# Kernel tuning notes

Measured on AMD Instinct MI355X. Metric: run time of the kernel, lower is better.

## Reference

```python
import jax, jax.numpy as jnp
import numpy as np

B, L, K, D, S = 8, 1024, 1024, 128, 16  # batch, nodes, eigvecs, d_model(=d_inner), d_state
ABAR_EPS = 1e-3
BN_EPS = 1e-5


def setup_inputs() -> dict:
    key = jax.random.key(0)
    ks = jax.random.split(key, 10)
    x = jax.random.normal(ks[0], (B, L, D), jnp.float32)
    attn_mask = jnp.ones((B, L), jnp.bool_)
    EigVecs = jax.random.normal(ks[1], (B, L, K), jnp.float32)
    EigVals = jax.random.uniform(ks[2], (B, K), jnp.float32)
    # BatchNorm1d (eval mode) params
    bn_gamma = jnp.ones((D,), jnp.float32)
    bn_beta = jnp.zeros((D,), jnp.float32)
    bn_mean = jnp.zeros((D,), jnp.float32)
    bn_var = jnp.ones((D,), jnp.float32)
    # in_proj Linear(D, 2*D)
    W_in = jax.random.normal(ks[3], (D, 2 * D), jnp.float32) / np.float32(np.sqrt(D))
    b_in = jnp.zeros((2 * D,), jnp.float32)
    # SSM params
    log_Delta = np.float32(np.log(1e-3)) + np.float32(np.log(0.1) - np.log(1e-3)) * jax.random.uniform(ks[4], (1, D), jnp.float32)
    Bp = 0.01 * jax.random.normal(ks[5], (1, D, S), jnp.float32)
    Cp = 0.01 * jax.random.normal(ks[6], (1, D, S), jnp.float32)
    log_A_real = jnp.log(0.5 * jnp.ones((D, S), jnp.float32))
    A_imag = jnp.pi * jnp.broadcast_to(jnp.arange(D, dtype=jnp.float32)[:, None], (D, S))
    # out_proj Linear(D, D)
    W_out = jax.random.normal(ks[7], (D, D), jnp.float32) / np.float32(np.sqrt(D))
    b_out = jnp.zeros((D,), jnp.float32)
    return {
        "x": x, "attn_mask": attn_mask, "EigVecs": EigVecs, "EigVals": EigVals,
        "bn_gamma": bn_gamma, "bn_beta": bn_beta, "bn_mean": bn_mean, "bn_var": bn_var,
        "W_in": W_in, "b_in": b_in, "log_Delta": log_Delta, "Bp": Bp, "Cp": Cp,
        "log_A_real": log_A_real, "A_imag": A_imag, "W_out": W_out, "b_out": b_out,
    }


def reference(x, attn_mask, EigVecs, EigVals, bn_gamma, bn_beta, bn_mean, bn_var,
              W_in, b_in, log_Delta, Bp, Cp, log_A_real, A_imag, W_out, b_out):
    # --- eig preprocessing ---
    ev = 1.0 - EigVals[:, :, None, None]            # (B,K,1,1)
    ev = jnp.nan_to_num(ev)
    Q = jnp.nan_to_num(EigVecs)                      # (B,L,K)
    Q = Q / jnp.linalg.norm(Q, axis=-1, keepdims=True)
    Q = jnp.nan_to_num(Q)
    # --- in_proj: BatchNorm1d (eval) + Linear ---
    xb = (x - bn_mean) * (bn_gamma / jnp.sqrt(bn_var + BN_EPS)) + bn_beta
    h = xb @ W_in + b_in                             # (B,L,2D)
    x1, z = jnp.split(h, 2, axis=-1)                 # split [d_model, d_model]
    u = x1 * jax.nn.silu(z)                          # (B,L,D)
    # --- discretized SSM params ---
    delta = jnp.exp(log_Delta)                       # (1,D)
    A = -jnp.exp(log_A_real) + 1j * A_imag           # (D,S) complex
    Abar = jnp.exp(-ABAR_EPS + delta[..., None] * A) # (1,D,S) complex
    Bbar = delta[..., None] * Bp                     # (1,D,S)
    # --- graph Fourier transform ---
    QTX = jnp.einsum('blk,bld->bkd', Q, u)           # (B,K,D)
    QTXB = QTX[..., None] * Bbar                     # (B,K,D,S)
    lamA = ev * Abar[:, None]                        # (B,K,D,S) complex
    lamQ = jnp.real(lamA / (1.0 - lamA) * QTXB)      # A_complex & not BC_complex -> .real
    # --- inverse transform + C reduction (fused) ---
    yssm = jnp.einsum('blk,bkds,ds->bld', Q, lamQ, Cp[0])  # (B,L,D)
    y = jax.nn.silu(yssm) @ W_out + b_out
    return y
```

## Files before the change

kernel.cpp:

```cpp
#include <hip/hip_runtime.h>
#include <math.h>

#define B_ 8
#define L_ 1024
#define K_ 1024
#define D_ 128
#define S_ 16
#define DS_ (D_ * S_)
#define NIT_ 16

typedef short bf16x8 __attribute__((ext_vector_type(8)));
typedef float f32x4 __attribute__((ext_vector_type(4)));
typedef __attribute__((address_space(1))) const unsigned int gu32;
typedef __attribute__((address_space(3))) unsigned int lu32;

__device__ inline unsigned short f2bf(float f) {
    unsigned int u = __float_as_uint(f);
    u = (u + 0x7fffu + ((u >> 16) & 1u)) >> 16;
    return (unsigned short)u;
}
__device__ inline float bf2f(unsigned short h) {
    return __uint_as_float(((unsigned int)h) << 16);
}

__device__ inline size_t bswz(int b, int c, int n) {
    return ((((size_t)b * 32 + (c >> 5)) * 4 + ((c >> 3) & 3)) * 128 + n) * 8;
}

__global__ __launch_bounds__(256) void k_w(
    const float* __restrict__ W_in,
    unsigned short* __restrict__ wiH, unsigned short* __restrict__ wiL) {
    int g = blockIdx.x * 256 + threadIdx.x;
    int lane = g & 63, rest = g >> 6;
    int ct = rest & 3, wv = (rest >> 2) & 3, c = rest >> 4;
    int rbase = c * 32 + (lane >> 4) * 8;
    int col = wv * 64 + ct * 16 + (lane & 15);
    bf16x8 hv, lv;
    #pragma unroll
    for (int i = 0; i < 8; ++i) {
        float wvl = W_in[(rbase + i) * 256 + col];
        unsigned short h = f2bf(wvl);
        hv[i] = (short)h;
        lv[i] = (short)f2bf(wvl - bf2f(h));
    }
    *(bf16x8*)&wiH[(size_t)g * 8] = hv;
    *(bf16x8*)&wiL[(size_t)g * 8] = lv;
}

__global__ __launch_bounds__(256) void k_pre(
    const float* __restrict__ E, const float* __restrict__ x,
    const float* __restrict__ g, const float* __restrict__ beta,
    const float* __restrict__ mean, const float* __restrict__ var,
    const unsigned short* __restrict__ wiH, const unsigned short* __restrict__ wiL,
    const float* __restrict__ b_in,
    const float* __restrict__ log_Delta, const float* __restrict__ Bp,
    const float* __restrict__ Cp, const float* __restrict__ log_A_real,
    const float* __restrict__ A_imag, const float* __restrict__ W_out,
    float* __restrict__ rn_out, float* __restrict__ par,
    unsigned short* __restrict__ woH, unsigned short* __restrict__ woL,
    unsigned short* __restrict__ uswH, unsigned short* __restrict__ uswL) {
    __shared__ unsigned short xbh[4][16][32], xbl[4][16][32];
    __shared__ float szs[16][132];
    __shared__ float us[16][132];
    __shared__ float rsum[16];
    __shared__ float rnS[16];
    int bx = blockIdx.x;
    int row0 = bx * 16;
    int t = threadIdx.x;
    if (bx < 8) {
        int i = bx * 256 + t;
        int d = i >> 4, s = i & 15;
        double delta = exp((double)log_Delta[d]);
        double Are = -exp((double)log_A_real[i]);
        double Aim = (double)A_imag[i];
        double mag = exp(-1e-3 + delta * Are);
        double ang = delta * Aim;
        int o = s * D_ + d;
        par[o]           = (float)(mag * cos(ang));
        par[DS_ + o]     = (float)(mag * sin(ang));
        par[2 * DS_ + o] = (float)(delta * (double)Bp[i] * (double)Cp[i]);
    }
    if (bx >= 8 && bx < 12) {
        int kc = bx - 8;
        #pragma unroll
        for (int j = 0; j < 16; ++j) {
            int s = t * 16 + j;
            int ws = s >> 10, nt = (s >> 9) & 1, ln = (s >> 3) & 63, ii = s & 7;
            int row = kc * 32 + (ln >> 4) * 8 + ii;
            int col = ws * 32 + nt * 16 + (ln & 15);
            float wv = W_out[row * 128 + col];
            unsigned short h = f2bf(wv);
            woH[kc * 4096 + s] = h;
            woL[kc * 4096 + s] = f2bf(wv - bf2f(h));
        }
    }
    {
        int r = t >> 4, tt = t & 15;
        const float4* Ep = (const float4*)(E + (size_t)(row0 + r) * K_);
        float s = 0.f;
        #pragma unroll
        for (int i = 0; i < 16; ++i) {
            float4 v = Ep[tt + i * 16];
            s += v.x * v.x + v.y * v.y + v.z * v.z + v.w * v.w;
        }
        s += __shfl_xor(s, 8, 64);
        s += __shfl_xor(s, 4, 64);
        s += __shfl_xor(s, 2, 64);
        s += __shfl_xor(s, 1, 64);
        if (tt == 0) rsum[r] = s;
    }
    #pragma unroll
    for (int p = 0; p < 8; ++p) {
        int idx = t + p * 256;
        int dd = idx & 127, r = idx >> 7;
        float sc = g[dd] / sqrtf(var[dd] + 1e-5f);
        float v = (x[(size_t)(row0 + r) * D_ + dd] - mean[dd]) * sc + beta[dd];
        unsigned short h = f2bf(v);
        xbh[dd >> 5][r][dd & 31] = h;
        xbl[dd >> 5][r][dd & 31] = f2bf(v - bf2f(h));
    }
    __syncthreads();
    if (t < 16) {
        float rv = 1.0f / sqrtf(rsum[t]);
        rnS[t] = rv;
        rn_out[row0 + t] = rv;
    }
    __syncthreads();
    int wave = t >> 6, lane = t & 63;
    int fr = lane & 15, q = lane >> 4;
    const bf16x8* WIH = (const bf16x8*)wiH;
    const bf16x8* WIL = (const bf16x8*)wiL;
    f32x4 acc[4];
    #pragma unroll
    for (int ct = 0; ct < 4; ++ct) acc[ct] = (f32x4){0.f, 0.f, 0.f, 0.f};
    #pragma unroll
    for (int c = 0; c < 4; ++c) {
        bf16x8 ah = *(const bf16x8*)&xbh[c][fr][q * 8];
        bf16x8 al = *(const bf16x8*)&xbl[c][fr][q * 8];
        #pragma unroll
        for (int ct = 0; ct < 4; ++ct) {
            int idx = ((c * 4 + wave) * 4 + ct) * 64 + lane;
            bf16x8 bh = WIH[idx];
            bf16x8 bl = WIL[idx];
            acc[ct] = __builtin_amdgcn_mfma_f32_16x16x32_bf16(ah, bh, acc[ct], 0, 0, 0);
            acc[ct] = __builtin_amdgcn_mfma_f32_16x16x32_bf16(ah, bl, acc[ct], 0, 0, 0);
            acc[ct] = __builtin_amdgcn_mfma_f32_16x16x32_bf16(al, bh, acc[ct], 0, 0, 0);
        }
    }
    if (wave >= 2) {
        #pragma unroll
        for (int ct = 0; ct < 4; ++ct) {
            int cz = (wave - 2) * 64 + ct * 16 + fr;
            float b2v = b_in[128 + cz];
            #pragma unroll
            for (int r = 0; r < 4; ++r) {
                float z = acc[ct][r] + b2v;
                float sig = 1.0f / (1.0f + __expf(-z));
                szs[q * 4 + r][cz] = z * sig;
            }
        }
    }
    __syncthreads();
    if (wave < 2) {
        #pragma unroll
        for (int ct = 0; ct < 4; ++ct) {
            int cx = wave * 64 + ct * 16 + fr;
            float b1v = b_in[cx];
            #pragma unroll
            for (int r = 0; r < 4; ++r) {
                int row = q * 4 + r;
                float x1 = acc[ct][r] + b1v;
                us[row][cx] = rnS[row] * x1 * szs[row][cx];
            }
        }
    }
    __syncthreads();
    int j = t & 127, half = t >> 7;
    bf16x8 hv, lv;
    #pragma unroll
    for (int r = 0; r < 8; ++r) {
        float uv = us[half * 8 + r][j];
        unsigned short h = f2bf(uv);
        hv[r] = (short)h;
        lv[r] = (short)f2bf(uv - bf2f(h));
    }
    int b = row0 >> 10;
    int l0 = (row0 & 1023) + half * 8;
    size_t off = bswz(b, l0, j);
    *(bf16x8*)&uswH[off] = hv;
    *(bf16x8*)&uswL[off] = lv;
}

#define STAGE_B(itS, nb)                                                        \
    _Pragma("unroll")                                                           \
    for (int j2 = 0; j2 < 4; ++j2) {                                            \
        int s = wave * 4 + j2;                         \
        int cts = s >> 4, s2 = s & 15;                                          \
        int qq = s2 & 3, nh = (s2 >> 2) & 1, hl = s2 >> 3;                      \
        size_t src0 = (size_t)((itS) * 2 + cts) * 4096;                         \
        const unsigned short* src =                                             \
            (hl ? BbL : BbH) + src0 + ((size_t)qq * 128 + nh * 64 + lane) * 8;  \
        unsigned short* dst =                                                   \
            (hl ? &sBl[nb][cts][0] : &sBh[nb][cts][0]) + qq * 1032 + nh * 512;  \
        __builtin_amdgcn_global_load_lds((gu32*)src, (lu32*)dst, 16, 0, 0);     \
    }

#define G1_WRITE_A(nb, v0, v1, v2, v3)                                           \
    {                                                                            \
        unsigned short h0 = f2bf(v0), h1 = f2bf(v1);                             \
        unsigned short l0 = f2bf((v0) - bf2f(h0)), l1 = f2bf((v1) - bf2f(h1));   \
        *(unsigned int*)&sAh[nb][0][aoff] = (unsigned)h0 | ((unsigned)h1 << 16); \
        *(unsigned int*)&sAl[nb][0][aoff] = (unsigned)l0 | ((unsigned)l1 << 16); \
        unsigned short h2 = f2bf(v2), h3 = f2bf(v3);                             \
        unsigned short l2 = f2bf((v2) - bf2f(h2)), l3 = f2bf((v3) - bf2f(h3));   \
        *(unsigned int*)&sAh[nb][1][aoff] = (unsigned)h2 | ((unsigned)h3 << 16); \
        *(unsigned int*)&sAl[nb][1][aoff] = (unsigned)l2 | ((unsigned)l3 << 16); \
    }

#define MFMA_PHASE(aB, cB)                                                       \
    {                                                                            \
        __builtin_amdgcn_s_setprio(1);                                           \
        bf16x8 ah[2], al[2], bh[2], bl[2];                                       \
        _Pragma("unroll")                                                        \
        for (int mt = 0; mt < 2; ++mt) {                                         \
            int row = mt * 16 + fr;                                              \
            int p = (q + (row >> 3)) & 3;                                        \
            int offA = row * 40 + p * 8;                                         \
            ah[mt] = *(const bf16x8*)&sAh[aB][kh][offA];                         \
            al[mt] = *(const bf16x8*)&sAl[aB][kh][offA];                         \
        }                                                                        \
        _Pragma("unroll")                                                        \
        for (int nt = 0; nt < 2; ++nt) {                                         \
            int offB = q * 1032 + (wn + nt * 16 + fr) * 8;                       \
            bh[nt] = *(const bf16x8*)&sBh[cB][kh][offB];                         \
            bl[nt] = *(const bf16x8*)&sBl[cB][kh][offB];                         \
        }                                                                        \
        _Pragma("unroll")                                                        \
        for (int mt = 0; mt < 2; ++mt)                                           \
            _Pragma("unroll")                                                    \
            for (int nt = 0; nt < 2; ++nt) {                                     \
                acc[mt][nt] = __builtin_amdgcn_mfma_f32_16x16x32_bf16(ah[mt], bh[nt], acc[mt][nt], 0, 0, 0); \
                acc[mt][nt] = __builtin_amdgcn_mfma_f32_16x16x32_bf16(ah[mt], bl[nt], acc[mt][nt], 0, 0, 0); \
                acc[mt][nt] = __builtin_amdgcn_mfma_f32_16x16x32_bf16(al[mt], bh[nt], acc[mt][nt], 0, 0, 0); \
            }                                                                    \
        __builtin_amdgcn_s_setprio(0);                                           \
    }

__global__ __launch_bounds__(512, 2) void k_g1(
    const float* __restrict__ E,
    const unsigned short* __restrict__ BH, const unsigned short* __restrict__ BL,
    const float* __restrict__ EigVals, const float* __restrict__ par,
    unsigned short* __restrict__ GswH, unsigned short* __restrict__ GswL) {
    __shared__ alignas(16) unsigned short sAh[2][2][1280], sAl[2][2][1280];
    __shared__ alignas(16) unsigned short sBh[3][2][4128], sBl[3][2][4128];
    __shared__ float evS[32];
    int bx = blockIdx.x;
    int b = bx & 7;
    int m0 = (bx >> 3) * 32;
    const float* Ab = E + (size_t)b * (1024 * 1024);
    const unsigned short* BbH = BH + (size_t)b * 131072;
    const unsigned short* BbL = BL + (size_t)b * 131072;
    int t = threadIdx.x;
    int wave = t >> 6, lane = t & 63;
    int fr = lane & 15, q = lane >> 4;
    int kh = wave & 1;
    int wn = (wave >> 1) * 32;
    int am = t & 31, jj = t >> 5;
    int ag = jj >> 2;
    int arot = (ag + (am >> 3)) & 3;
    int aoff = am * 40 + arot * 8 + ((2 * jj) & 7);
    if (t < 32) evS[t] = 1.0f - EigVals[b * 1024 + m0 + t];
    f32x4 acc[2][2];
    #pragma unroll
    for (int mt = 0; mt < 2; ++mt)
        #pragma unroll
        for (int nt = 0; nt < 2; ++nt)
            acc[mt][nt] = (f32x4){0.f, 0.f, 0.f, 0.f};

    {
        STAGE_B(0, 0);
        STAGE_B(1, 1);
        float v0 = Ab[(size_t)(2 * jj) * 1024 + m0 + am];
        float v1 = Ab[(size_t)(2 * jj + 1) * 1024 + m0 + am];
        float v2 = Ab[(size_t)(32 + 2 * jj) * 1024 + m0 + am];
        float v3 = Ab[(size_t)(32 + 2 * jj + 1) * 1024 + m0 + am];
        G1_WRITE_A(0, v0, v1, v2, v3);
        asm volatile("s_waitcnt vmcnt(0) lgkmcnt(0)" ::: "memory");
        __builtin_amdgcn_s_barrier();
        asm volatile("" ::: "memory");
    }

    for (int it = 0; it < NIT_; ++it) {
        int cB = it % 3;
        int fB = (it + 2) % 3;
        int aB = it & 1, naB = aB ^ 1;
        float v0 = 0.f, v1 = 0.f, v2 = 0.f, v3 = 0.f;
        if (it + 1 < NIT_) {
            int cb = (it + 1) * 64;
            v0 = Ab[(size_t)(cb + 2 * jj) * 1024 + m0 + am];
            v1 = Ab[(size_t)(cb + 2 * jj + 1) * 1024 + m0 + am];
            v2 = Ab[(size_t)(cb + 32 + 2 * jj) * 1024 + m0 + am];
            v3 = Ab[(size_t)(cb + 32 + 2 * jj + 1) * 1024 + m0 + am];
        }
        if (it + 2 < NIT_) STAGE_B(it + 2, fB);
        MFMA_PHASE(aB, cB)
        if (it + 1 < NIT_) G1_WRITE_A(naB, v0, v1, v2, v3);
        asm volatile("s_waitcnt lgkmcnt(0)" ::: "memory");
        __builtin_amdgcn_s_barrier();
        asm volatile("" ::: "memory");
    }

    float (*Gs)[132] = (float (*)[132])(&sBh[0][0][0]);
    if (kh == 0) {
        #pragma unroll
        for (int mt = 0; mt < 2; ++mt)
            #pragma unroll
            for (int nt = 0; nt < 2; ++nt) {
                int col = wn + nt * 16 + fr;
                #pragma unroll
                for (int r = 0; r < 4; ++r)
                    Gs[mt * 16 + q * 4 + r][col] = acc[mt][nt][r];
            }
    }
    __syncthreads();
    if (kh == 1) {
        #pragma unroll
        for (int mt = 0; mt < 2; ++mt)
            #pragma unroll
            for (int nt = 0; nt < 2; ++nt) {
                int col = wn + nt * 16 + fr;
                #pragma unroll
                for (int r = 0; r < 4; ++r)
                    Gs[mt * 16 + q * 4 + r][col] += acc[mt][nt][r];
            }
    }
    __syncthreads();
    {
        int col = t & 127, rowg = t >> 7;
        float arr[S_], aii[S_], ccc[S_];
        #pragma unroll
        for (int ss = 0; ss < S_; ++ss) {
            arr[ss] = par[ss * D_ + col];
            aii[ss] = par[DS_ + ss * D_ + col];
            ccc[ss] = par[2 * DS_ + ss * D_ + col];
        }
        #pragma unroll
        for (int i = 0; i < 8; ++i) {
            int row = rowg * 8 + i;
            float ev = evS[row];
            float w = 0.f;
            #pragma unroll
            for (int sp = 0; sp < 8; ++sp) {
                float n0, n1, d0, d1;
                {
                    int ss = sp * 2;
                    float a = ev * arr[ss], bi = ev * aii[ss];
                    float oma = 1.0f - a;
                    d0 = fmaf(oma, oma, bi * bi);
                    n0 = ccc[ss] * (oma - d0);
                }
                {
                    int ss = sp * 2 + 1;
                    float a = ev * arr[ss], bi = ev * aii[ss];
                    float oma = 1.0f - a;
                    d1 = fmaf(oma, oma, bi * bi);
                    n1 = ccc[ss] * (oma - d1);
                }
                float num = fmaf(n0, d1, n1 * d0);
                float dpr = d0 * d1;
                float rr = __builtin_amdgcn_rcpf(dpr);
                rr = rr * (2.0f - dpr * rr);
                w = fmaf(num, rr, w);
            }
            Gs[row][col] *= w;
        }
    }
    __syncthreads();
    {
        int d = t & 127, kg = t >> 7;
        bf16x8 hv, lv;
        #pragma unroll
        for (int i = 0; i < 8; ++i) {
            float v = Gs[kg * 8 + i][d];
            unsigned short h = f2bf(v);
            hv[i] = (short)h;
            lv[i] = (short)f2bf(v - bf2f(h));
        }
        int ct = m0 >> 5;
        size_t off = (((size_t)(b * 32 + ct) * 4 + kg) * 128 + d) * 8;
        *(bf16x8*)&GswH[off] = hv;
        *(bf16x8*)&GswL[off] = lv;
    }
}

#define G2_WRITE_A(nb, va)                                                       \
    {                                                                            \
        unsigned short h0 = f2bf((va).x), h1 = f2bf((va).y);                     \
        unsigned short h2 = f2bf((va).z), h3 = f2bf((va).w);                     \
        unsigned short l0 = f2bf((va).x - bf2f(h0)), l1 = f2bf((va).y - bf2f(h1));\
        unsigned short l2 = f2bf((va).z - bf2f(h2)), l3 = f2bf((va).w - bf2f(h3));\
        *(uint2*)&sAh[nb][chunk][aoff] =                                         \
            (uint2){(unsigned)h0 | ((unsigned)h1 << 16),                         \
                    (unsigned)h2 | ((unsigned)h3 << 16)};                        \
        *(uint2*)&sAl[nb][chunk][aoff] =                                         \
            (uint2){(unsigned)l0 | ((unsigned)l1 << 16),                         \
                    (unsigned)l2 | ((unsigned)l3 << 16)};                        \
    }

__global__ __launch_bounds__(512, 2) void k_g2(
    const float* __restrict__ E,
    const unsigned short* __restrict__ BH, const unsigned short* __restrict__ BL,
    const float* __restrict__ rn,
    const unsigned short* __restrict__ woH, const unsigned short* __restrict__ woL,
    const float* __restrict__ b_out, float* __restrict__ y) {
    __shared__ alignas(16) unsigned short sAh[2][2][1280], sAl[2][2][1280];
    __shared__ alignas(16) unsigned short sBh[3][2][4128], sBl[3][2][4128];
    __shared__ float rnS[32];
    int bx = blockIdx.x;
    int b = bx & 7;
    int m0 = (bx >> 3) * 32;
    const float* Ab = E + (size_t)b * (1024 * 1024);
    const unsigned short* BbH = BH + (size_t)b * 131072;
    const unsigned short* BbL = BL + (size_t)b * 131072;
    int t = threadIdx.x;
    int wave = t >> 6, lane = t & 63;
    int fr = lane & 15, q = lane >> 4;
    int kh = wave & 1;
    int wn = (wave >> 1) * 32;
    int am = t >> 4, c4 = (t & 15) * 4;
    int chunk = c4 >> 5, cw = c4 & 31;
    int ag = cw >> 3;
    int arot = (ag + (am >> 3)) & 3;
    int aoff = am * 40 + arot * 8 + (cw & 7);
    if (t < 32) rnS[t] = rn[b * 1024 + m0 + t];
    f32x4 acc[2][2];
    #pragma unroll
    for (int mt = 0; mt < 2; ++mt)
        #pragma unroll
        for (int nt = 0; nt < 2; ++nt)
            acc[mt][nt] = (f32x4){0.f, 0.f, 0.f, 0.f};

    {
        STAGE_B(0, 0);
        STAGE_B(1, 1);
        float4 va = *(const float4*)&Ab[(size_t)(m0 + am) * 1024 + c4];
        G2_WRITE_A(0, va);
        asm volatile("s_waitcnt vmcnt(0) lgkmcnt(0)" ::: "memory");
        __builtin_amdgcn_s_barrier();
        asm volatile("" ::: "memory");
    }

    for (int it = 0; it < NIT_; ++it) {
        int cB = it % 3;
        int fB = (it + 2) % 3;
        int aB = it & 1, naB = aB ^ 1;
        float4 va = (float4){0.f, 0.f, 0.f, 0.f};
        if (it + 1 < NIT_)
            va = *(const float4*)&Ab[(size_t)(m0 + am) * 1024 + (it + 1) * 64 + c4];
        if (it + 2 < NIT_) STAGE_B(it + 2, fB);
        MFMA_PHASE(aB, cB)
        if (it + 1 < NIT_) G2_WRITE_A(naB, va);
        asm volatile("s_waitcnt lgkmcnt(0)" ::: "memory");
        __builtin_amdgcn_s_barrier();
        asm volatile("" ::: "memory");
    }

    float (*Ysf)[132] = (float (*)[132])(&sBh[0][0][0]);
    if (kh == 0) {
        #pragma unroll
        for (int mt = 0; mt < 2; ++mt)
            #pragma unroll
            for (int nt = 0; nt < 2; ++nt) {
                int col = wn + nt * 16 + fr;
                #pragma unroll
                for (int r = 0; r < 4; ++r)
                    Ysf[mt * 16 + q * 4 + r][col] = acc[mt][nt][r];
            }
    }
    __syncthreads();
    if (kh == 1) {
        #pragma unroll
        for (int mt = 0; mt < 2; ++mt)
            #pragma unroll
            for (int nt = 0; nt < 2; ++nt) {
                int col = wn + nt * 16 + fr;
                #pragma unroll
                for (int r = 0; r < 4; ++r)
                    Ysf[mt * 16 + q * 4 + r][col] += acc[mt][nt][r];
            }
    }
    __syncthreads();
    unsigned short (*ysh)[32][40] = (unsigned short (*)[32][40])(&sBl[0][0][0]);
    unsigned short (*ysl)[32][40] = (unsigned short (*)[32][40])(&sBl[0][0][0] + 5120);
    {
        int col = t & 127, rowg = t >> 7;
        #pragma unroll
        for (int i = 0; i < 8; ++i) {
            int row = rowg * 8 + i;
            float v = Ysf[row][col] * rnS[row];
            float sig = 1.0f / (1.0f + __expf(-v));
            float u = v * sig;
            unsigned short h = f2bf(u);
            ysh[col >> 5][row][col & 31] = h;
            ysl[col >> 5][row][col & 31] = f2bf(u - bf2f(h));
        }
    }
    __syncthreads();
    {
        int mh = wave & 1, ws = wave >> 1;
        const bf16x8* WH = (const bf16x8*)woH;
        const bf16x8* WL = (const bf16x8*)woL;
        f32x4 a2[2];
        a2[0] = (f32x4){0.f, 0.f, 0.f, 0.f};
        a2[1] = (f32x4){0.f, 0.f, 0.f, 0.f};
        #pragma unroll
        for (int kc = 0; kc < 4; ++kc) {
            bf16x8 ah = *(const bf16x8*)&ysh[kc][mh * 16 + fr][q * 8];
            bf16x8 al = *(const bf16x8*)&ysl[kc][mh * 16 + fr][q * 8];
            #pragma unroll
            for (int nt = 0; nt < 2; ++nt) {
                bf16x8 bh = WH[((kc * 4 + ws) * 2 + nt) * 64 + lane];
                bf16x8 bl = WL[((kc * 4 + ws) * 2 + nt) * 64 + lane];
                a2[nt] = __builtin_amdgcn_mfma_f32_16x16x32_bf16(ah, bh, a2[nt], 0, 0, 0);
                a2[nt] = __builtin_amdgcn_mfma_f32_16x16x32_bf16(ah, bl, a2[nt], 0, 0, 0);
                a2[nt] = __builtin_amdgcn_mfma_f32_16x16x32_bf16(al, bh, a2[nt], 0, 0, 0);
            }
        }
        #pragma unroll
        for (int nt = 0; nt < 2; ++nt) {
            int col = ws * 32 + nt * 16 + fr;
            float bo = b_out[col];
            #pragma unroll
            for (int r = 0; r < 4; ++r) {
                int row = mh * 16 + q * 4 + r;
                y[((size_t)b * 1024 + m0 + row) * 128 + col] = a2[nt][r] + bo;
            }
        }
    }
}

extern "C" void kernel_launch(void* const* d_in, const int* in_sizes, int n_in,
                              void* d_out, int out_size, void* d_ws, size_t ws_size,
                              hipStream_t stream) {
    const float* x          = (const float*)d_in[0];
    const float* EigVecs    = (const float*)d_in[2];
    const float* EigVals    = (const float*)d_in[3];
    const float* bn_gamma   = (const float*)d_in[4];
    const float* bn_beta    = (const float*)d_in[5];
    const float* bn_mean    = (const float*)d_in[6];
    const float* bn_var     = (const float*)d_in[7];
    const float* W_in       = (const float*)d_in[8];
    const float* b_in       = (const float*)d_in[9];
    const float* log_Delta  = (const float*)d_in[10];
    const float* Bp         = (const float*)d_in[11];
    const float* Cp         = (const float*)d_in[12];
    const float* log_A_real = (const float*)d_in[13];
    const float* A_imag     = (const float*)d_in[14];
    const float* W_out      = (const float*)d_in[15];
    const float* b_out      = (const float*)d_in[16];

    float* y = (float*)d_out;
    char* w = (char*)d_ws;
    float* rn            = (float*)(w);
    float* par           = (float*)(w + 32768);
    unsigned short* woH  = (unsigned short*)(w + 57344);
    unsigned short* woL  = (unsigned short*)(w + 90112);
    unsigned short* wiH  = (unsigned short*)(w + 131072);
    unsigned short* wiL  = (unsigned short*)(w + 196608);
    unsigned short* uswH = (unsigned short*)(w + 262144);
    unsigned short* uswL = (unsigned short*)(w + 262144 + (1u << 21));
    unsigned short* GswH = (unsigned short*)(w + 262144 + 2 * (1u << 21));
    unsigned short* GswL = (unsigned short*)(w + 262144 + 3 * (1u << 21));

    k_w<<<dim3(16), dim3(256), 0, stream>>>(W_in, wiH, wiL);
    k_pre<<<dim3(B_ * L_ / 16), dim3(256), 0, stream>>>(
        EigVecs, x, bn_gamma, bn_beta, bn_mean, bn_var, wiH, wiL, b_in,
        log_Delta, Bp, Cp, log_A_real, A_imag, W_out, rn, par, woH, woL,
        uswH, uswL);
    k_g1<<<dim3(256), dim3(512), 0, stream>>>(
        EigVecs, uswH, uswL, EigVals, par, GswH, GswL);
    k_g2<<<dim3(256), dim3(512), 0, stream>>>(
        EigVecs, GswH, GswL, rn, woH, woL, b_out, y);
}
```

Baseline: 152.3 us.

## Merge the two GEMM kernels into one cooperative kernel with a grid sync

Fuses k_g1 (the forward graph transform plus spectral filter) and k_g2 (the inverse transform plus out_proj) into a single cooperative kernel. A grid-wide barrier separates the two phases. The first A tile of the second phase is prefetched before the barrier. The aim is to remove one kernel launch and its drain/fill gap and to hide some load latency. In exchange it adds the cost of a grid sync, and it relies on all 256 blocks of 512 threads being co-resident.

```diff
diff --git a/kernel.cpp b/kernel.cpp
--- a/kernel.cpp
+++ b/kernel.cpp
@@ -1,5 +1,8 @@
 #include <hip/hip_runtime.h>
+#include <hip/hip_cooperative_groups.h>
 #include <math.h>
+
+namespace cg = cooperative_groups;
 
 #define B_ 8
 #define L_ 1024
@@ -246,153 +249,6 @@
         __builtin_amdgcn_s_setprio(0);                                           \
     }
 
-__global__ __launch_bounds__(512, 2) void k_g1(
-    const float* __restrict__ E,
-    const unsigned short* __restrict__ BH, const unsigned short* __restrict__ BL,
-    const float* __restrict__ EigVals, const float* __restrict__ par,
-    unsigned short* __restrict__ GswH, unsigned short* __restrict__ GswL) {
-    __shared__ alignas(16) unsigned short sAh[2][2][1280], sAl[2][2][1280];
-    __shared__ alignas(16) unsigned short sBh[3][2][4128], sBl[3][2][4128];
-    __shared__ float evS[32];
-    int bx = blockIdx.x;
-    int b = bx & 7;
-    int m0 = (bx >> 3) * 32;
-    const float* Ab = E + (size_t)b * (1024 * 1024);
-    const unsigned short* BbH = BH + (size_t)b * 131072;
-    const unsigned short* BbL = BL + (size_t)b * 131072;
-    int t = threadIdx.x;
-    int wave = t >> 6, lane = t & 63;
-    int fr = lane & 15, q = lane >> 4;
-    int kh = wave & 1;
-    int wn = (wave >> 1) * 32;
-    int am = t & 31, jj = t >> 5;
-    int ag = jj >> 2;
-    int arot = (ag + (am >> 3)) & 3;
-    int aoff = am * 40 + arot * 8 + ((2 * jj) & 7);
-    if (t < 32) evS[t] = 1.0f - EigVals[b * 1024 + m0 + t];
-    f32x4 acc[2][2];
-    #pragma unroll
-    for (int mt = 0; mt < 2; ++mt)
-        #pragma unroll
-        for (int nt = 0; nt < 2; ++nt)
-            acc[mt][nt] = (f32x4){0.f, 0.f, 0.f, 0.f};
-
-    {
-        STAGE_B(0, 0);
-        STAGE_B(1, 1);
-        float v0 = Ab[(size_t)(2 * jj) * 1024 + m0 + am];
-        float v1 = Ab[(size_t)(2 * jj + 1) * 1024 + m0 + am];
-        float v2 = Ab[(size_t)(32 + 2 * jj) * 1024 + m0 + am];
-        float v3 = Ab[(size_t)(32 + 2 * jj + 1) * 1024 + m0 + am];
-        G1_WRITE_A(0, v0, v1, v2, v3);
-        asm volatile("s_waitcnt vmcnt(0) lgkmcnt(0)" ::: "memory");
-        __builtin_amdgcn_s_barrier();
-        asm volatile("" ::: "memory");
-    }
-
-    for (int it = 0; it < NIT_; ++it) {
-        int cB = it % 3;
-        int fB = (it + 2) % 3;
-        int aB = it & 1, naB = aB ^ 1;
-        float v0 = 0.f, v1 = 0.f, v2 = 0.f, v3 = 0.f;
-        if (it + 1 < NIT_) {
-            int cb = (it + 1) * 64;
-            v0 = Ab[(size_t)(cb + 2 * jj) * 1024 + m0 + am];
-            v1 = Ab[(size_t)(cb + 2 * jj + 1) * 1024 + m0 + am];
-            v2 = Ab[(size_t)(cb + 32 + 2 * jj) * 1024 + m0 + am];
-            v3 = Ab[(size_t)(cb + 32 + 2 * jj + 1) * 1024 + m0 + am];
-        }
-        if (it + 2 < NIT_) STAGE_B(it + 2, fB);
-        MFMA_PHASE(aB, cB)
-        if (it + 1 < NIT_) G1_WRITE_A(naB, v0, v1, v2, v3);
-        asm volatile("s_waitcnt lgkmcnt(0)" ::: "memory");
-        __builtin_amdgcn_s_barrier();
-        asm volatile("" ::: "memory");
-    }
-
-    float (*Gs)[132] = (float (*)[132])(&sBh[0][0][0]);
-    if (kh == 0) {
-        #pragma unroll
-        for (int mt = 0; mt < 2; ++mt)
-            #pragma unroll
-            for (int nt = 0; nt < 2; ++nt) {
-                int col = wn + nt * 16 + fr;
-                #pragma unroll
-                for (int r = 0; r < 4; ++r)
-                    Gs[mt * 16 + q * 4 + r][col] = acc[mt][nt][r];
-            }
-    }
-    __syncthreads();
-    if (kh == 1) {
-        #pragma unroll
-        for (int mt = 0; mt < 2; ++mt)
-            #pragma unroll
-            for (int nt = 0; nt < 2; ++nt) {
-                int col = wn + nt * 16 + fr;
-                #pragma unroll
-                for (int r = 0; r < 4; ++r)
-                    Gs[mt * 16 + q * 4 + r][col] += acc[mt][nt][r];
-            }
-    }
-    __syncthreads();
-    {
-        int col = t & 127, rowg = t >> 7;
-        float arr[S_], aii[S_], ccc[S_];
-        #pragma unroll
-        for (int ss = 0; ss < S_; ++ss) {
-            arr[ss] = par[ss * D_ + col];
-            aii[ss] = par[DS_ + ss * D_ + col];
-            ccc[ss] = par[2 * DS_ + ss * D_ + col];
-        }
-        #pragma unroll
-        for (int i = 0; i < 8; ++i) {
-            int row = rowg * 8 + i;
-            float ev = evS[row];
-            float w = 0.f;
-            #pragma unroll
-            for (int sp = 0; sp < 8; ++sp) {
-                float n0, n1, d0, d1;
-                {
-                    int ss = sp * 2;
-                    float a = ev * arr[ss], bi = ev * aii[ss];
-                    float oma = 1.0f - a;
-                    d0 = fmaf(oma, oma, bi * bi);
-                    n0 = ccc[ss] * (oma - d0);
-                }
-                {
-                    int ss = sp * 2 + 1;
-                    float a = ev * arr[ss], bi = ev * aii[ss];
-                    float oma = 1.0f - a;
-                    d1 = fmaf(oma, oma, bi * bi);
-                    n1 = ccc[ss] * (oma - d1);
-                }
-                float num = fmaf(n0, d1, n1 * d0);
-                float dpr = d0 * d1;
-                float rr = __builtin_amdgcn_rcpf(dpr);
-                rr = rr * (2.0f - dpr * rr);
-                w = fmaf(num, rr, w);
-            }
-            Gs[row][col] *= w;
-        }
-    }
-    __syncthreads();
-    {
-        int d = t & 127, kg = t >> 7;
-        bf16x8 hv, lv;
-        #pragma unroll
-        for (int i = 0; i < 8; ++i) {
-            float v = Gs[kg * 8 + i][d];
-            unsigned short h = f2bf(v);
-            hv[i] = (short)h;
-            lv[i] = (short)f2bf(v - bf2f(h));
-        }
-        int ct = m0 >> 5;
-        size_t off = (((size_t)(b * 32 + ct) * 4 + kg) * 128 + d) * 8;
-        *(bf16x8*)&GswH[off] = hv;
-        *(bf16x8*)&GswL[off] = lv;
-    }
-}
-
 #define G2_WRITE_A(nb, va)                                                       \
     {                                                                            \
         unsigned short h0 = f2bf((va).x), h1 = f2bf((va).y);                     \
@@ -407,133 +263,275 @@
                     (unsigned)l2 | ((unsigned)l3 << 16)};                        \
     }
 
-__global__ __launch_bounds__(512, 2) void k_g2(
+__global__ __launch_bounds__(512, 2) void k_gg(
     const float* __restrict__ E,
-    const unsigned short* __restrict__ BH, const unsigned short* __restrict__ BL,
+    const unsigned short* __restrict__ uswH, const unsigned short* __restrict__ uswL,
+    const float* __restrict__ EigVals, const float* __restrict__ par,
+    unsigned short* __restrict__ GswH, unsigned short* __restrict__ GswL,
     const float* __restrict__ rn,
     const unsigned short* __restrict__ woH, const unsigned short* __restrict__ woL,
     const float* __restrict__ b_out, float* __restrict__ y) {
     __shared__ alignas(16) unsigned short sAh[2][2][1280], sAl[2][2][1280];
     __shared__ alignas(16) unsigned short sBh[3][2][4128], sBl[3][2][4128];
+    __shared__ float evS[32];
     __shared__ float rnS[32];
     int bx = blockIdx.x;
     int b = bx & 7;
     int m0 = (bx >> 3) * 32;
     const float* Ab = E + (size_t)b * (1024 * 1024);
-    const unsigned short* BbH = BH + (size_t)b * 131072;
-    const unsigned short* BbL = BL + (size_t)b * 131072;
     int t = threadIdx.x;
     int wave = t >> 6, lane = t & 63;
     int fr = lane & 15, q = lane >> 4;
     int kh = wave & 1;
     int wn = (wave >> 1) * 32;
-    int am = t >> 4, c4 = (t & 15) * 4;
-    int chunk = c4 >> 5, cw = c4 & 31;
-    int ag = cw >> 3;
-    int arot = (ag + (am >> 3)) & 3;
-    int aoff = am * 40 + arot * 8 + (cw & 7);
+
+    {
+        const unsigned short* BbH = uswH + (size_t)b * 131072;
+        const unsigned short* BbL = uswL + (size_t)b * 131072;
+        int am = t & 31, jj = t >> 5;
+        int ag = jj >> 2;
+        int arot = (ag + (am >> 3)) & 3;
+        int aoff = am * 40 + arot * 8 + ((2 * jj) & 7);
+        if (t < 32) evS[t] = 1.0f - EigVals[b * 1024 + m0 + t];
+        f32x4 acc[2][2];
+        #pragma unroll
+        for (int mt = 0; mt < 2; ++mt)
+            #pragma unroll
+            for (int nt = 0; nt < 2; ++nt)
+                acc[mt][nt] = (f32x4){0.f, 0.f, 0.f, 0.f};
+
+        {
+            STAGE_B(0, 0);
+            STAGE_B(1, 1);
+            float v0 = Ab[(size_t)(2 * jj) * 1024 + m0 + am];
+            float v1 = Ab[(size_t)(2 * jj + 1) * 1024 + m0 + am];
+            float v2 = Ab[(size_t)(32 + 2 * jj) * 1024 + m0 + am];
+            float v3 = Ab[(size_t)(32 + 2 * jj + 1) * 1024 + m0 + am];
+            G1_WRITE_A(0, v0, v1, v2, v3);
+            asm volatile("s_waitcnt vmcnt(0) lgkmcnt(0)" ::: "memory");
+            __builtin_amdgcn_s_barrier();
+            asm volatile("" ::: "memory");
+        }
+
+        for (int it = 0; it < NIT_; ++it) {
+            int cB = it % 3;
+            int fB = (it + 2) % 3;
+            int aB = it & 1, naB = aB ^ 1;
+            float v0 = 0.f, v1 = 0.f, v2 = 0.f, v3 = 0.f;
+            if (it + 1 < NIT_) {
+                int cb = (it + 1) * 64;
+                v0 = Ab[(size_t)(cb + 2 * jj) * 1024 + m0 + am];
+                v1 = Ab[(size_t)(cb + 2 * jj + 1) * 1024 + m0 + am];
+                v2 = Ab[(size_t)(cb + 32 + 2 * jj) * 1024 + m0 + am];
+                v3 = Ab[(size_t)(cb + 32 + 2 * jj + 1) * 1024 + m0 + am];
+            }
+            if (it + 2 < NIT_) STAGE_B(it + 2, fB);
+            MFMA_PHASE(aB, cB)
+            if (it + 1 < NIT_) G1_WRITE_A(naB, v0, v1, v2, v3);
+            asm volatile("s_waitcnt lgkmcnt(0)" ::: "memory");
+            __builtin_amdgcn_s_barrier();
+            asm volatile("" ::: "memory");
+        }
+
+        float (*Gs)[132] = (float (*)[132])(&sBh[0][0][0]);
+        if (kh == 0) {
+            #pragma unroll
+            for (int mt = 0; mt < 2; ++mt)
+                #pragma unroll
+                for (int nt = 0; nt < 2; ++nt) {
+                    int col = wn + nt * 16 + fr;
+                    #pragma unroll
+                    for (int r = 0; r < 4; ++r)
+                        Gs[mt * 16 + q * 4 + r][col] = acc[mt][nt][r];
+                }
+        }
+        __syncthreads();
+        if (kh == 1) {
+            #pragma unroll
+            for (int mt = 0; mt < 2; ++mt)
+                #pragma unroll
+                for (int nt = 0; nt < 2; ++nt) {
+                    int col = wn + nt * 16 + fr;
+                    #pragma unroll
+                    for (int r = 0; r < 4; ++r)
+                        Gs[mt * 16 + q * 4 + r][col] += acc[mt][nt][r];
+                }
+        }
+        __syncthreads();
+        {
+            int col = t & 127, rowg = t >> 7;
+            float arr[S_], aii[S_], ccc[S_];
+            #pragma unroll
+            for (int ss = 0; ss < S_; ++ss) {
+                arr[ss] = par[ss * D_ + col];
+                aii[ss] = par[DS_ + ss * D_ + col];
+                ccc[ss] = par[2 * DS_ + ss * D_ + col];
+            }
+            #pragma unroll
+            for (int i = 0; i < 8; ++i) {
+                int row = rowg * 8 + i;
+                float ev = evS[row];
+                float w = 0.f;
+                #pragma unroll
+                for (int sp = 0; sp < 8; ++sp) {
+                    float n0, n1, d0, d1;
+                    {
+                        int ss = sp * 2;
+                        float a = ev * arr[ss], bi = ev * aii[ss];
+                        float oma = 1.0f - a;
+                        d0 = fmaf(oma, oma, bi * bi);
+                        n0 = ccc[ss] * (oma - d0);
+                    }
+                    {
+                        int ss = sp * 2 + 1;
+                        float a = ev * arr[ss], bi = ev * aii[ss];
+                        float oma = 1.0f - a;
+                        d1 = fmaf(oma, oma, bi * bi);
+                        n1 = ccc[ss] * (oma - d1);
+                    }
+                    float num = fmaf(n0, d1, n1 * d0);
+                    float dpr = d0 * d1;
+                    float rr = __builtin_amdgcn_rcpf(dpr);
+                    rr = rr * (2.0f - dpr * rr);
+                    w = fmaf(num, rr, w);
+                }
+                Gs[row][col] *= w;
+            }
+        }
+        __syncthreads();
+        {
+            int d = t & 127, kg = t >> 7;
+            bf16x8 hv, lv;
+            #pragma unroll
+            for (int i = 0; i < 8; ++i) {
+                float v = Gs[kg * 8 + i][d];
+                unsigned short h = f2bf(v);
+                hv[i] = (short)h;
+                lv[i] = (short)f2bf(v - bf2f(h));
+            }
+            int ct = m0 >> 5;
+            size_t off = (((size_t)(b * 32 + ct) * 4 + kg) * 128 + d) * 8;
+            *(bf16x8*)&GswH[off] = hv;
+            *(bf16x8*)&GswL[off] = lv;
+        }
+    }
+
+    int am2 = t >> 4, c42 = (t & 15) * 4;
+    float4 va0 = *(const float4*)&Ab[(size_t)(m0 + am2) * 1024 + c42];
     if (t < 32) rnS[t] = rn[b * 1024 + m0 + t];
-    f32x4 acc[2][2];
-    #pragma unroll
-    for (int mt = 0; mt < 2; ++mt)
-        #pragma unroll
-        for (int nt = 0; nt < 2; ++nt)
-            acc[mt][nt] = (f32x4){0.f, 0.f, 0.f, 0.f};
+
+    __threadfence();
+    cg::this_grid().sync();
 
     {
-        STAGE_B(0, 0);
-        STAGE_B(1, 1);
-        float4 va = *(const float4*)&Ab[(size_t)(m0 + am) * 1024 + c4];
-        G2_WRITE_A(0, va);
-        asm volatile("s_waitcnt vmcnt(0) lgkmcnt(0)" ::: "memory");
-        __builtin_amdgcn_s_barrier();
-        asm volatile("" ::: "memory");
-    }
-
-    for (int it = 0; it < NIT_; ++it) {
-        int cB = it % 3;
-        int fB = (it + 2) % 3;
-        int aB = it & 1, naB = aB ^ 1;
-        float4 va = (float4){0.f, 0.f, 0.f, 0.f};
-        if (it + 1 < NIT_)
-            va = *(const float4*)&Ab[(size_t)(m0 + am) * 1024 + (it + 1) * 64 + c4];
-        if (it + 2 < NIT_) STAGE_B(it + 2, fB);
-        MFMA_PHASE(aB, cB)
-        if (it + 1 < NIT_) G2_WRITE_A(naB, va);
-        asm volatile("s_waitcnt lgkmcnt(0)" ::: "memory");
-        __builtin_amdgcn_s_barrier();
-        asm volatile("" ::: "memory");
-    }
-
-    float (*Ysf)[132] = (float (*)[132])(&sBh[0][0][0]);
-    if (kh == 0) {
+        const unsigned short* BbH = GswH + (size_t)b * 131072;
+        const unsigned short* BbL = GswL + (size_t)b * 131072;
+        int am = am2, c4 = c42;
+        int chunk = c4 >> 5, cw = c4 & 31;
+        int ag = cw >> 3;
+        int arot = (ag + (am >> 3)) & 3;
+        int aoff = am * 40 + arot * 8 + (cw & 7);
+        f32x4 acc[2][2];
         #pragma unroll
         for (int mt = 0; mt < 2; ++mt)
             #pragma unroll
+            for (int nt = 0; nt < 2; ++nt)
+                acc[mt][nt] = (f32x4){0.f, 0.f, 0.f, 0.f};
+
+        {
+            STAGE_B(0, 0);
+            STAGE_B(1, 1);
+            G2_WRITE_A(0, va0);
+            asm volatile("s_waitcnt vmcnt(0) lgkmcnt(0)" ::: "memory");
+            __builtin_amdgcn_s_barrier();
+            asm volatile("" ::: "memory");
+        }
+
+        for (int it = 0; it < NIT_; ++it) {
+            int cB = it % 3;
+            int fB = (it + 2) % 3;
+            int aB = it & 1, naB = aB ^ 1;
+            float4 va = (float4){0.f, 0.f, 0.f, 0.f};
+            if (it + 1 < NIT_)
+                va = *(const float4*)&Ab[(size_t)(m0 + am) * 1024 + (it + 1) * 64 + c4];
+            if (it + 2 < NIT_) STAGE_B(it + 2, fB);
+            MFMA_PHASE(aB, cB)
+            if (it + 1 < NIT_) G2_WRITE_A(naB, va);
+            asm volatile("s_waitcnt lgkmcnt(0)" ::: "memory");
+            __builtin_amdgcn_s_barrier();
+            asm volatile("" ::: "memory");
+        }
+
+        float (*Ysf)[132] = (float (*)[132])(&sBh[0][0][0]);
+        if (kh == 0) {
+            #pragma unroll
+            for (int mt = 0; mt < 2; ++mt)
+                #pragma unroll
+                for (int nt = 0; nt < 2; ++nt) {
+                    int col = wn + nt * 16 + fr;
+                    #pragma unroll
+                    for (int r = 0; r < 4; ++r)
+                        Ysf[mt * 16 + q * 4 + r][col] = acc[mt][nt][r];
+                }
+        }
+        __syncthreads();
+        if (kh == 1) {
+            #pragma unroll
+            for (int mt = 0; mt < 2; ++mt)
+                #pragma unroll
+                for (int nt = 0; nt < 2; ++nt) {
+                    int col = wn + nt * 16 + fr;
+                    #pragma unroll
+                    for (int r = 0; r < 4; ++r)
+                        Ysf[mt * 16 + q * 4 + r][col] += acc[mt][nt][r];
+                }
+        }
+        __syncthreads();
+        unsigned short (*ysh)[32][40] = (unsigned short (*)[32][40])(&sBl[0][0][0]);
+        unsigned short (*ysl)[32][40] = (unsigned short (*)[32][40])(&sBl[0][0][0] + 5120);
+        {
+            int col = t & 127, rowg = t >> 7;
+            #pragma unroll
+            for (int i = 0; i < 8; ++i) {
+                int row = rowg * 8 + i;
+                float v = Ysf[row][col] * rnS[row];
+                float sig = 1.0f / (1.0f + __expf(-v));
+                float u = v * sig;
+                unsigned short h = f2bf(u);
+                ysh[col >> 5][row][col & 31] = h;
+                ysl[col >> 5][row][col & 31] = f2bf(u - bf2f(h));
+            }
+        }
+        __syncthreads();
+        {
+            int mh = wave & 1, ws = wave >> 1;
+            const bf16x8* WH = (const bf16x8*)woH;
+            const bf16x8* WL = (const bf16x8*)woL;
+            f32x4 a2[2];
+            a2[0] = (f32x4){0.f, 0.f, 0.f, 0.f};
+            a2[1] = (f32x4){0.f, 0.f, 0.f, 0.f};
+            #pragma unroll
+            for (int kc = 0; kc < 4; ++kc) {
+                bf16x8 ah = *(const bf16x8*)&ysh[kc][mh * 16 + fr][q * 8];
+                bf16x8 al = *(const bf16x8*)&ysl[kc][mh * 16 + fr][q * 8];
+                #pragma unroll
+                for (int nt = 0; nt < 2; ++nt) {
+                    bf16x8 bh = WH[((kc * 4 + ws) * 2 + nt) * 64 + lane];
+                    bf16x8 bl = WL[((kc * 4 + ws) * 2 + nt) * 64 + lane];
+                    a2[nt] = __builtin_amdgcn_mfma_f32_16x16x32_bf16(ah, bh, a2[nt], 0, 0, 0);
+                    a2[nt] = __builtin_amdgcn_mfma_f32_16x16x32_bf16(ah, bl, a2[nt], 0, 0, 0);
+                    a2[nt] = __builtin_amdgcn_mfma_f32_16x16x32_bf16(al, bh, a2[nt], 0, 0, 0);
+                }
+            }
+            #pragma unroll
             for (int nt = 0; nt < 2; ++nt) {
-                int col = wn + nt * 16 + fr;
-                #pragma unroll
-                for (int r = 0; r < 4; ++r)
-                    Ysf[mt * 16 + q * 4 + r][col] = acc[mt][nt][r];
-            }
-    }
-    __syncthreads();
-    if (kh == 1) {
-        #pragma unroll
-        for (int mt = 0; mt < 2; ++mt)
-            #pragma unroll
-            for (int nt = 0; nt < 2; ++nt) {
-                int col = wn + nt * 16 + fr;
-                #pragma unroll
-                for (int r = 0; r < 4; ++r)
-                    Ysf[mt * 16 + q * 4 + r][col] += acc[mt][nt][r];
-            }
-    }
-    __syncthreads();
-    unsigned short (*ysh)[32][40] = (unsigned short (*)[32][40])(&sBl[0][0][0]);
-    unsigned short (*ysl)[32][40] = (unsigned short (*)[32][40])(&sBl[0][0][0] + 5120);
-    {
-        int col = t & 127, rowg = t >> 7;
-        #pragma unroll
-        for (int i = 0; i < 8; ++i) {
-            int row = rowg * 8 + i;
-            float v = Ysf[row][col] * rnS[row];
-            float sig = 1.0f / (1.0f + __expf(-v));
-            float u = v * sig;
-            unsigned short h = f2bf(u);
-            ysh[col >> 5][row][col & 31] = h;
-            ysl[col >> 5][row][col & 31] = f2bf(u - bf2f(h));
-        }
-    }
-    __syncthreads();
-    {
-        int mh = wave & 1, ws = wave >> 1;
-        const bf16x8* WH = (const bf16x8*)woH;
-        const bf16x8* WL = (const bf16x8*)woL;
-        f32x4 a2[2];
-        a2[0] = (f32x4){0.f, 0.f, 0.f, 0.f};
-        a2[1] = (f32x4){0.f, 0.f, 0.f, 0.f};
-        #pragma unroll
-        for (int kc = 0; kc < 4; ++kc) {
-            bf16x8 ah = *(const bf16x8*)&ysh[kc][mh * 16 + fr][q * 8];
-            bf16x8 al = *(const bf16x8*)&ysl[kc][mh * 16 + fr][q * 8];
-            #pragma unroll
-            for (int nt = 0; nt < 2; ++nt) {
-                bf16x8 bh = WH[((kc * 4 + ws) * 2 + nt) * 64 + lane];
-                bf16x8 bl = WL[((kc * 4 + ws) * 2 + nt) * 64 + lane];
-                a2[nt] = __builtin_amdgcn_mfma_f32_16x16x32_bf16(ah, bh, a2[nt], 0, 0, 0);
-                a2[nt] = __builtin_amdgcn_mfma_f32_16x16x32_bf16(ah, bl, a2[nt], 0, 0, 0);
-                a2[nt] = __builtin_amdgcn_mfma_f32_16x16x32_bf16(al, bh, a2[nt], 0, 0, 0);
-            }
-        }
-        #pragma unroll
-        for (int nt = 0; nt < 2; ++nt) {
-            int col = ws * 32 + nt * 16 + fr;
-            float bo = b_out[col];
-            #pragma unroll
-            for (int r = 0; r < 4; ++r) {
-                int row = mh * 16 + q * 4 + r;
-                y[((size_t)b * 1024 + m0 + row) * 128 + col] = a2[nt][r] + bo;
+                int col = ws * 32 + nt * 16 + fr;
+                float bo = b_out[col];
+                #pragma unroll
+                for (int r = 0; r < 4; ++r) {
+                    int row = mh * 16 + q * 4 + r;
+                    y[((size_t)b * 1024 + m0 + row) * 128 + col] = a2[nt][r] + bo;
+                }
             }
         }
     }
@@ -577,8 +575,23 @@
         EigVecs, x, bn_gamma, bn_beta, bn_mean, bn_var, wiH, wiL, b_in,
         log_Delta, Bp, Cp, log_A_real, A_imag, W_out, rn, par, woH, woL,
         uswH, uswL);
-    k_g1<<<dim3(256), dim3(512), 0, stream>>>(
-        EigVecs, uswH, uswL, EigVals, par, GswH, GswL);
-    k_g2<<<dim3(256), dim3(512), 0, stream>>>(
-        EigVecs, GswH, GswL, rn, woH, woL, b_out, y);
-}
+    {
+        const float* E_ = EigVecs;
+        const unsigned short* BH_ = uswH;
+        const unsigned short* BL_ = uswL;
+        const float* EV_ = EigVals;
+        const float* par_ = par;
+        unsigned short* GH_ = GswH;
+        unsigned short* GL_ = GswL;
+        const float* rn_ = rn;
+        const unsigned short* WH_ = woH;
+        const unsigned short* WL_ = woL;
+        const float* bo_ = b_out;
+        float* y_ = y;
+        void* args[] = {(void*)&E_, (void*)&BH_, (void*)&BL_, (void*)&EV_,
+                        (void*)&par_, (void*)&GH_, (void*)&GL_, (void*)&rn_,
+                        (void*)&WH_, (void*)&WL_, (void*)&bo_, (void*)&y_};
+        hipLaunchCooperativeKernel((const void*)k_gg, dim3(256), dim3(512),
+                                   args, 0, stream);
+    }
+}
```

Result: slower. 260.6 us (+71.1%).
